# Kernel optimization log

Measured on AMD Instinct MI355X. Metric: run time of the kernel, lower is better.

Reference implementation:

```python
import jax, jax.numpy as jnp
import numpy as np

N_QUBITS = 5
Q_DEPTH = 1
HALF_PI = np.pi / 2.0

H_GATE = (1.0 / np.sqrt(2.0)) * jnp.array([[1, 1], [1, -1]], dtype=jnp.complex64)
CNOT = jnp.array([[1, 0, 0, 0],
                  [0, 1, 0, 0],
                  [0, 0, 0, 1],
                  [0, 0, 1, 0]], dtype=jnp.complex64).reshape(2, 2, 2, 2)


def _apply_1q(state, gate, wire):
    # state: (2,)*N_QUBITS complex, gate: (2,2) complex
    state = jnp.tensordot(gate, state, axes=([1], [wire]))
    return jnp.moveaxis(state, 0, wire)


def _apply_cnot(state, control, target):
    state = jnp.tensordot(CNOT, state, axes=([2, 3], [control, target]))
    return jnp.moveaxis(state, (0, 1), (control, target))


def _ry(t):
    c = jnp.cos(t / 2).astype(jnp.complex64)
    s = jnp.sin(t / 2).astype(jnp.complex64)
    return jnp.stack([jnp.stack([c, -s]), jnp.stack([s, c])])


def _rx(t):
    c = jnp.cos(t / 2).astype(jnp.complex64)
    js = (-1j) * jnp.sin(t / 2).astype(jnp.complex64)
    return jnp.stack([jnp.stack([c, js]), jnp.stack([js, c])])


def _circuit(angles, q_weights):
    # angles: (N_QUBITS,), q_weights: (Q_DEPTH, N_QUBITS)
    state = jnp.zeros((2,) * N_QUBITS, dtype=jnp.complex64).at[(0,) * N_QUBITS].set(1.0)
    for w in range(N_QUBITS):
        state = _apply_1q(state, H_GATE, w)
    for w in range(N_QUBITS):
        state = _apply_1q(state, _ry(angles[w]), w)
    for k in range(Q_DEPTH):
        # BasicEntanglerLayers: RX rotations then ring of CNOTs
        for w in range(N_QUBITS):
            state = _apply_1q(state, _rx(q_weights[k, w]), w)
        for w in range(N_QUBITS):
            state = _apply_cnot(state, w, (w + 1) % N_QUBITS)
    probs = state.real ** 2 + state.imag ** 2
    zvals = []
    for w in range(N_QUBITS):
        p = probs.sum(axis=tuple(i for i in range(N_QUBITS) if i != w))  # (2,)
        zvals.append(p[0] - p[1])
    return jnp.stack(zvals)  # (N_QUBITS,)


def setup_inputs() -> dict:
    key = jax.random.key(0)
    k1, k2, k3, k4, k5, k6 = jax.random.split(key, 6)
    B = 65536
    return {
        "input_features": jax.random.normal(k1, (B, 512), dtype=jnp.float32),
        "w_pre": jax.random.normal(k2, (N_QUBITS, 512), dtype=jnp.float32) * 0.04,
        "b_pre": jax.random.normal(k3, (N_QUBITS,), dtype=jnp.float32) * 0.04,
        "q_params": 0.01 * jax.random.uniform(k4, (Q_DEPTH * N_QUBITS,), dtype=jnp.float32),
        "w_post": jax.random.normal(k5, (2, N_QUBITS), dtype=jnp.float32) * 0.4,
        "b_post": jax.random.normal(k6, (2,), dtype=jnp.float32) * 0.4,
    }


def reference(input_features, w_pre, b_pre, q_params, w_post, b_post):
    pre_out = input_features @ w_pre.T + b_pre            # (B, 5)
    q_in = jnp.tanh(pre_out) * HALF_PI                    # (B, 5)
    q_weights = q_params.reshape(Q_DEPTH, N_QUBITS)
    q_out = jax.vmap(lambda a: _circuit(a, q_weights))(q_in)  # (B, 5) real
    q_out = q_out.astype(jnp.float32)
    return q_out @ w_post.T + b_post                      # (B, 2)
```

## Files before the change

kernel.cpp:

```cpp
#include <hip/hip_runtime.h>
#include <math.h>

#define NQ 5
#define D 512
#define R 4
#define HALF_PI 1.57079632679489662f

typedef float f32x4 __attribute__((ext_vector_type(4)));


#define DPP_ADD(v, CTRL)                                                        \
    ((v) + __builtin_bit_cast(float, __builtin_amdgcn_update_dpp(               \
               0, __builtin_bit_cast(int, (v)), (CTRL), 0xF, 0xF, true)))

__device__ __forceinline__ float wave_sum(float v) {
    v = DPP_ADD(v, 0xB1);
    v = DPP_ADD(v, 0x4E);
    v = DPP_ADD(v, 0x141);
    v = DPP_ADD(v, 0x140);
    int vi = __builtin_amdgcn_ds_swizzle(__builtin_bit_cast(int, v), 0x401F);
    v = v + __builtin_bit_cast(float, vi);
    const int vb = __builtin_bit_cast(int, v);
    const float lo = __builtin_bit_cast(float, __builtin_amdgcn_readlane(vb, 0));
    const float hi = __builtin_bit_cast(float, __builtin_amdgcn_readlane(vb, 32));
    return lo + hi;
}

__global__ __launch_bounds__(256) void dressed_qnet_kernel(
    const float* __restrict__ x,
    const float* __restrict__ w_pre,
    const float* __restrict__ b_pre,
    const float* __restrict__ q_params,
    const float* __restrict__ w_post,
    const float* __restrict__ b_post,
    float* __restrict__ out,
    int B)
{
    const int lane = threadIdx.x & 63;
    const int wave = (blockIdx.x * blockDim.x + threadIdx.x) >> 6;
    const int row0 = wave * R;
    if (row0 >= B) return;

    f32x4 xa[R], xb[R];
#pragma unroll
    for (int r = 0; r < R; ++r) {
        const int row = (row0 + r < B) ? (row0 + r) : (B - 1);
        const f32x4* xr = reinterpret_cast<const f32x4*>(x + (size_t)row * D);
        xa[r] = __builtin_nontemporal_load(xr + lane);
        xb[r] = __builtin_nontemporal_load(xr + lane + 64);
    }

    f32x4 w0[NQ], w1[NQ];
#pragma unroll
    for (int q = 0; q < NQ; ++q) {
        w0[q] = *reinterpret_cast<const f32x4*>(w_pre + q * D + lane * 4);
        w1[q] = *reinterpret_cast<const f32x4*>(w_pre + q * D + 256 + lane * 4);
    }

    float bp[NQ], ct[NQ], wp0[NQ], wp1[NQ];
#pragma unroll
    for (int q = 0; q < NQ; ++q) {
        bp[q]  = b_pre[q];
        ct[q]  = __cosf(q_params[q]);
        wp0[q] = w_post[q];
        wp1[q] = w_post[NQ + q];
    }
    const float bpost0 = b_post[0];
    const float bpost1 = b_post[1];

    float acc[R][NQ];
#pragma unroll
    for (int r = 0; r < R; ++r) {
#pragma unroll
        for (int q = 0; q < NQ; ++q) {
            float s;
            s = xa[r].x * w0[q].x;
            s = fmaf(xa[r].y, w0[q].y, s);
            s = fmaf(xa[r].z, w0[q].z, s);
            s = fmaf(xa[r].w, w0[q].w, s);
            s = fmaf(xb[r].x, w1[q].x, s);
            s = fmaf(xb[r].y, w1[q].y, s);
            s = fmaf(xb[r].z, w1[q].z, s);
            s = fmaf(xb[r].w, w1[q].w, s);
            acc[r][q] = s;
        }
    }

#pragma unroll
    for (int r = 0; r < R; ++r)
#pragma unroll
        for (int q = 0; q < NQ; ++q)
            acc[r][q] = wave_sum(acc[r][q]);

    float o[R][2];
#pragma unroll
    for (int r = 0; r < R; ++r) {
        float z[NQ];
#pragma unroll
        for (int q = 0; q < NQ; ++q) {
            const float p = acc[r][q] + bp[q];
            const float e = __expf(2.0f * p);
            const float th = 1.0f - 2.0f / (e + 1.0f);
            z[q] = -__sinf(HALF_PI * th) * ct[q];
        }
        const float v1   = z[0] * z[1];
        const float z234 = z[2] * z[3] * z[4];
        const float v0   = z[1] * z234;
        const float v2   = v1 * z[2];
        const float v3   = v2 * z[3];
        const float v4   = v1 * z234;

        float o0 = bpost0, o1 = bpost1;
        o0 = fmaf(wp0[0], v0, o0); o1 = fmaf(wp1[0], v0, o1);
        o0 = fmaf(wp0[1], v1, o0); o1 = fmaf(wp1[1], v1, o1);
        o0 = fmaf(wp0[2], v2, o0); o1 = fmaf(wp1[2], v2, o1);
        o0 = fmaf(wp0[3], v3, o0); o1 = fmaf(wp1[3], v3, o1);
        o0 = fmaf(wp0[4], v4, o0); o1 = fmaf(wp1[4], v4, o1);
        o[r][0] = o0; o[r][1] = o1;
    }

    if (lane == 0) {
        if (row0 + R <= B) {
            f32x4* dst = reinterpret_cast<f32x4*>(out + (size_t)row0 * 2);
            f32x4 d0 = { o[0][0], o[0][1], o[1][0], o[1][1] };
            f32x4 d1 = { o[2][0], o[2][1], o[3][0], o[3][1] };
            dst[0] = d0;
            dst[1] = d1;
        } else {
#pragma unroll
            for (int r = 0; r < R; ++r)
                if (row0 + r < B) {
                    out[(size_t)(row0 + r) * 2 + 0] = o[r][0];
                    out[(size_t)(row0 + r) * 2 + 1] = o[r][1];
                }
        }
    }
}

extern "C" void kernel_launch(void* const* d_in, const int* in_sizes, int n_in,
                              void* d_out, int out_size, void* d_ws, size_t ws_size,
                              hipStream_t stream) {
    const float* x        = (const float*)d_in[0];
    const float* w_pre    = (const float*)d_in[1];
    const float* b_pre    = (const float*)d_in[2];
    const float* q_params = (const float*)d_in[3];
    const float* w_post   = (const float*)d_in[4];
    const float* b_post   = (const float*)d_in[5];
    float* out = (float*)d_out;

    const int B = in_sizes[0] / D;

    const int threads = 256;
    const int rows_per_block = (threads / 64) * R;
    const int blocks = (B + rows_per_block - 1) / rows_per_block;
    dressed_qnet_kernel<<<blocks, threads, 0, stream>>>(
        x, w_pre, b_pre, q_params, w_post, b_post, out, B);
}
```

Baseline: 34.57 us.

## Switch to persistent grid-stride waves with register double-buffered row prefetch

Replaces the one-shot launch, where each wave handles four rows, with a fixed grid of 2048 blocks whose waves loop over pairs of rows. Each iteration prefetches the next pair into registers while the current pair is reduced and evaluated, aiming to overlap HBM loads with the wave reductions and math. The weights are loaded once per wave instead of once per four rows, and scalar constants are made wave-uniform via readfirstlane. Loads drop the nontemporal hint, and the tail handling now assumes B is even.

```diff
diff --git a/kernel.cpp b/kernel.cpp
--- a/kernel.cpp
+++ b/kernel.cpp
@@ -3,7 +3,6 @@
 
 #define NQ 5
 #define D 512
-#define R 4
 #define HALF_PI 1.57079632679489662f
 
 typedef float f32x4 __attribute__((ext_vector_type(4)));
@@ -26,7 +25,25 @@
     return lo + hi;
 }
 
-__global__ __launch_bounds__(256) void dressed_qnet_kernel(
+__device__ __forceinline__ float uni(float v) {
+    return __builtin_bit_cast(float,
+        __builtin_amdgcn_readfirstlane(__builtin_bit_cast(int, v)));
+}
+
+__device__ __forceinline__ float dot8(f32x4 a, f32x4 b, f32x4 c, f32x4 d) {
+    float s;
+    s = a.x * b.x;
+    s = fmaf(a.y, b.y, s);
+    s = fmaf(a.z, b.z, s);
+    s = fmaf(a.w, b.w, s);
+    s = fmaf(c.x, d.x, s);
+    s = fmaf(c.y, d.y, s);
+    s = fmaf(c.z, d.z, s);
+    s = fmaf(c.w, d.w, s);
+    return s;
+}
+
+__global__ __launch_bounds__(256, 4) void dressed_qnet_kernel(
     const float* __restrict__ x,
     const float* __restrict__ w_pre,
     const float* __restrict__ b_pre,
@@ -37,18 +54,15 @@
     int B)
 {
     const int lane = threadIdx.x & 63;
-    const int wave = (blockIdx.x * blockDim.x + threadIdx.x) >> 6;
-    const int row0 = wave * R;
+    const int wid  = (blockIdx.x * blockDim.x + threadIdx.x) >> 6;
+    const int nw   = (gridDim.x * blockDim.x) >> 6;
+    const int rstep = 2 * nw;
+
+    int row0 = 2 * wid;
     if (row0 >= B) return;
 
-    f32x4 xa[R], xb[R];
-#pragma unroll
-    for (int r = 0; r < R; ++r) {
-        const int row = (row0 + r < B) ? (row0 + r) : (B - 1);
-        const f32x4* xr = reinterpret_cast<const f32x4*>(x + (size_t)row * D);
-        xa[r] = __builtin_nontemporal_load(xr + lane);
-        xb[r] = __builtin_nontemporal_load(xr + lane + 64);
-    }
+    const f32x4* p0 = reinterpret_cast<const f32x4*>(x + (size_t)row0 * D);
+    f32x4 a0 = p0[lane], a1 = p0[lane + 64], b0 = p0[lane + 128], b1 = p0[lane + 192];
 
     f32x4 w0[NQ], w1[NQ];
 #pragma unroll
@@ -60,80 +74,70 @@
     float bp[NQ], ct[NQ], wp0[NQ], wp1[NQ];
 #pragma unroll
     for (int q = 0; q < NQ; ++q) {
-        bp[q]  = b_pre[q];
-        ct[q]  = __cosf(q_params[q]);
-        wp0[q] = w_post[q];
-        wp1[q] = w_post[NQ + q];
+        bp[q]  = uni(b_pre[q]);
+        ct[q]  = uni(__cosf(q_params[q]));
+        wp0[q] = uni(w_post[q]);
+        wp1[q] = uni(w_post[NQ + q]);
     }
-    const float bpost0 = b_post[0];
-    const float bpost1 = b_post[1];
+    const float bo0 = uni(b_post[0]);
+    const float bo1 = uni(b_post[1]);
 
-    float acc[R][NQ];
-#pragma unroll
-    for (int r = 0; r < R; ++r) {
+    for (; row0 < B; row0 += rstep) {
+        const int nrow = row0 + rstep;
+        f32x4 na0, na1, nb0, nb1;
+        if (nrow < B) {
+            const f32x4* pn = reinterpret_cast<const f32x4*>(x + (size_t)nrow * D);
+            na0 = pn[lane];
+            na1 = pn[lane + 64];
+            nb0 = pn[lane + 128];
+            nb1 = pn[lane + 192];
+        }
+
+        float acc[2][NQ];
 #pragma unroll
         for (int q = 0; q < NQ; ++q) {
-            float s;
-            s = xa[r].x * w0[q].x;
-            s = fmaf(xa[r].y, w0[q].y, s);
-            s = fmaf(xa[r].z, w0[q].z, s);
-            s = fmaf(xa[r].w, w0[q].w, s);
-            s = fmaf(xb[r].x, w1[q].x, s);
-            s = fmaf(xb[r].y, w1[q].y, s);
-            s = fmaf(xb[r].z, w1[q].z, s);
-            s = fmaf(xb[r].w, w1[q].w, s);
-            acc[r][q] = s;
+            acc[0][q] = dot8(a0, w0[q], a1, w1[q]);
+            acc[1][q] = dot8(b0, w0[q], b1, w1[q]);
         }
-    }
+#pragma unroll
+        for (int r = 0; r < 2; ++r)
+#pragma unroll
+            for (int q = 0; q < NQ; ++q)
+                acc[r][q] = wave_sum(acc[r][q]);
 
+        float o[2][2];
 #pragma unroll
-    for (int r = 0; r < R; ++r)
+        for (int r = 0; r < 2; ++r) {
+            float z[NQ];
 #pragma unroll
-        for (int q = 0; q < NQ; ++q)
-            acc[r][q] = wave_sum(acc[r][q]);
+            for (int q = 0; q < NQ; ++q) {
+                const float pv = acc[r][q] + bp[q];
+                const float e  = __expf(2.0f * pv);
+                const float th = 1.0f - 2.0f / (e + 1.0f);
+                z[q] = -__sinf(HALF_PI * th) * ct[q];
+            }
+            const float v1   = z[0] * z[1];
+            const float z234 = z[2] * z[3] * z[4];
+            const float v0   = z[1] * z234;
+            const float v2   = v1 * z[2];
+            const float v3   = v2 * z[3];
+            const float v4   = v1 * z234;
 
-    float o[R][2];
-#pragma unroll
-    for (int r = 0; r < R; ++r) {
-        float z[NQ];
-#pragma unroll
-        for (int q = 0; q < NQ; ++q) {
-            const float p = acc[r][q] + bp[q];
-            const float e = __expf(2.0f * p);
-            const float th = 1.0f - 2.0f / (e + 1.0f);
-            z[q] = -__sinf(HALF_PI * th) * ct[q];
+            float s0 = bo0, s1 = bo1;
+            s0 = fmaf(wp0[0], v0, s0); s1 = fmaf(wp1[0], v0, s1);
+            s0 = fmaf(wp0[1], v1, s0); s1 = fmaf(wp1[1], v1, s1);
+            s0 = fmaf(wp0[2], v2, s0); s1 = fmaf(wp1[2], v2, s1);
+            s0 = fmaf(wp0[3], v3, s0); s1 = fmaf(wp1[3], v3, s1);
+            s0 = fmaf(wp0[4], v4, s0); s1 = fmaf(wp1[4], v4, s1);
+            o[r][0] = s0; o[r][1] = s1;
         }
-        const float v1   = z[0] * z[1];
-        const float z234 = z[2] * z[3] * z[4];
-        const float v0   = z[1] * z234;
-        const float v2   = v1 * z[2];
-        const float v3   = v2 * z[3];
-        const float v4   = v1 * z234;
 
-        float o0 = bpost0, o1 = bpost1;
-        o0 = fmaf(wp0[0], v0, o0); o1 = fmaf(wp1[0], v0, o1);
-        o0 = fmaf(wp0[1], v1, o0); o1 = fmaf(wp1[1], v1, o1);
-        o0 = fmaf(wp0[2], v2, o0); o1 = fmaf(wp1[2], v2, o1);
-        o0 = fmaf(wp0[3], v3, o0); o1 = fmaf(wp1[3], v3, o1);
-        o0 = fmaf(wp0[4], v4, o0); o1 = fmaf(wp1[4], v4, o1);
-        o[r][0] = o0; o[r][1] = o1;
-    }
+        if (lane == 0) {
+            f32x4 dd = { o[0][0], o[0][1], o[1][0], o[1][1] };
+            *reinterpret_cast<f32x4*>(out + (size_t)row0 * 2) = dd;
+        }
 
-    if (lane == 0) {
-        if (row0 + R <= B) {
-            f32x4* dst = reinterpret_cast<f32x4*>(out + (size_t)row0 * 2);
-            f32x4 d0 = { o[0][0], o[0][1], o[1][0], o[1][1] };
-            f32x4 d1 = { o[2][0], o[2][1], o[3][0], o[3][1] };
-            dst[0] = d0;
-            dst[1] = d1;
-        } else {
-#pragma unroll
-            for (int r = 0; r < R; ++r)
-                if (row0 + r < B) {
-                    out[(size_t)(row0 + r) * 2 + 0] = o[r][0];
-                    out[(size_t)(row0 + r) * 2 + 1] = o[r][1];
-                }
-        }
+        a0 = na0; a1 = na1; b0 = nb0; b1 = nb1;
     }
 }
 
@@ -151,8 +155,7 @@
     const int B = in_sizes[0] / D;
 
     const int threads = 256;
-    const int rows_per_block = (threads / 64) * R;
-    const int blocks = (B + rows_per_block - 1) / rows_per_block;
+    const int blocks  = 2048;
     dressed_qnet_kernel<<<blocks, threads, 0, stream>>>(
         x, w_pre, b_pre, q_params, w_post, b_post, out, B);
 }
```

Result: no change. 34.60 us (+0.1%).
